# Kernel tuning notes

Measured on AMD Instinct MI355X. Metric: run time of the kernel, lower is better.

Reference implementation:

```python
import jax, jax.numpy as jnp
import numpy as np

B, T, N_EMBD = 1, 512, 768
N_HEAD, N_KV_HEAD = 12, 6
HEAD_DIM = N_EMBD // N_HEAD  # 64


def rms_norm(x, eps=1e-6):
    return x * jax.lax.rsqrt(jnp.mean(x * x, axis=-1, keepdims=True) + eps)


def apply_rotary_emb(x, cos, sin):
    # x: [B, T, H, D]; cos/sin: [T, D//2]
    d2 = x.shape[-1] // 2
    x1, x2 = x[..., :d2], x[..., d2:]
    c = cos[None, :, None, :]
    s = sin[None, :, None, :]
    return jnp.concatenate([x1 * c - x2 * s, x2 * c + x1 * s], axis=-1)


def tropical_dot_product(q, k):
    # q: [B,H,T,D], k: [B,H,S,D] -> max-plus score [B,H,T,S]
    return jnp.max(q[..., :, None, :] + k[..., None, :, :], axis=-1)


def setup_inputs() -> dict:
    key = jax.random.key(0)
    ks = jax.random.split(key, 5)
    x = jax.random.normal(ks[0], (B, T, N_EMBD), dtype=jnp.float32)
    # Real RoPE tables
    half = HEAD_DIM // 2
    inv_freq = 1.0 / (10000.0 ** (np.arange(0, half, dtype=np.float32) / half))
    t = np.arange(T, dtype=np.float32)
    freqs = np.outer(t, inv_freq)  # [T, D//2]
    cos = jnp.asarray(np.cos(freqs), dtype=jnp.float32)
    sin = jnp.asarray(np.sin(freqs), dtype=jnp.float32)
    std = 0.02
    Wq = std * jax.random.normal(ks[1], (N_EMBD, N_HEAD * HEAD_DIM), dtype=jnp.float32)
    Wk = std * jax.random.normal(ks[2], (N_EMBD, N_KV_HEAD * HEAD_DIM), dtype=jnp.float32)
    Wv = std * jax.random.normal(ks[3], (N_EMBD, N_KV_HEAD * HEAD_DIM), dtype=jnp.float32)
    Wproj = std * jax.random.normal(ks[4], (N_EMBD, N_EMBD), dtype=jnp.float32)
    return {"x": x, "cos": cos, "sin": sin, "Wq": Wq, "Wk": Wk, "Wv": Wv, "Wproj": Wproj}


def reference(x, cos, sin, Wq, Wk, Wv, Wproj):
    b, t, c = x.shape
    q = (x @ Wq).reshape(b, t, N_HEAD, HEAD_DIM)
    k = (x @ Wk).reshape(b, t, N_KV_HEAD, HEAD_DIM)
    v = (x @ Wv).reshape(b, t, N_KV_HEAD, HEAD_DIM)
    q = rms_norm(apply_rotary_emb(q, cos, sin))
    k = rms_norm(apply_rotary_emb(k, cos, sin))
    q = jnp.transpose(q, (0, 2, 1, 3))  # [B,H,T,D]
    k = jnp.transpose(k, (0, 2, 1, 3))  # [B,Hkv,T,D]
    v = jnp.transpose(v, (0, 2, 1, 3))
    n_rep = N_HEAD // N_KV_HEAD
    if n_rep > 1:
        k = jnp.repeat(k, n_rep, axis=1)
        v = jnp.repeat(v, n_rep, axis=1)
    scores = tropical_dot_product(q, k)  # [B,H,T,T]
    causal = jnp.tril(jnp.ones((t, t), dtype=jnp.bool_))
    scores = scores + jnp.where(causal, 0.0, -jnp.inf)
    attn = jax.nn.softmax(scores, axis=-1)
    y = jnp.einsum('bhqk,bhkd->bhqd', attn, v)
    y = jnp.transpose(y, (0, 2, 1, 3)).reshape(b, t, c)
    return y @ Wproj
```

## Files before the change

kernel.cpp:

```cpp
#include <hip/hip_runtime.h>
#include <hip/hip_bf16.h>
#include <math.h>

#define TT   512
#define CEMB 768
#define NH   12
#define NKV  6
#define HD   64
#define KVC  (NKV*HD)

typedef short short8 __attribute__((ext_vector_type(8)));
typedef float floatx4 __attribute__((ext_vector_type(4)));
typedef float floatx2 __attribute__((ext_vector_type(2)));

__device__ __forceinline__ unsigned pack_bf16(float lo, float hi){
  __hip_bfloat162 h = __float22bfloat162_rn(make_float2(lo, hi));
  return *reinterpret_cast<unsigned*>(&h);
}
__device__ __forceinline__ unsigned short bf16_rn(float f){
  unsigned u = __float_as_uint(f);
  u += 0x7FFFu + ((u>>16)&1u);
  return (unsigned short)(u>>16);
}
__device__ __forceinline__ float bf16_to_f32(unsigned short u){
  return __uint_as_float(((unsigned)u) << 16);
}

__global__ void __launch_bounds__(256) gemm_qkv_mfma(
    const float* __restrict__ X,
    const float* __restrict__ Wq, const float* __restrict__ Wk, const float* __restrict__ Wv,
    const float* __restrict__ Wp,
    const float* __restrict__ cosb, const float* __restrict__ sinb,
    float* __restrict__ q, float* __restrict__ k, float* __restrict__ v,
    unsigned short* __restrict__ WpF){
  int bx = blockIdx.x;
  if (bx >= 192){
    int t0 = (bx-192)*256 + threadIdx.x;
    for(int g=0; g<8; ++g){
      int u  = g*9216 + t0;
      int kp = u / 192;
      int n4 = (u - kp*192)*4;
      int kk = kp*2;
      float4 w0 = *(const float4*)&Wp[(size_t)kk*CEMB + n4];
      float4 w1 = *(const float4*)&Wp[(size_t)(kk+1)*CEMB + n4];
      int ks = kk>>5, qq = (kk>>3)&3, j = kk&7;
      #pragma unroll
      for(int i=0;i<4;i++){
        int n = n4+i, ct = n>>4, r = n&15;
        *(unsigned*)&WpF[ (((size_t)(ct*24 + ks)*64 + qq*16 + r)<<3) + j ] =
          pack_bf16((&w0.x)[i], (&w1.x)[i]);
      }
    }
    return;
  }
  int mt = bx / 24, nt = bx % 24;
  const float* W; int ldb, bcol;
  if (nt < 12)      { W = Wq; ldb = CEMB; bcol = nt*64; }
  else if (nt < 18) { W = Wk; ldb = KVC;  bcol = (nt-12)*64; }
  else              { W = Wv; ldb = KVC;  bcol = (nt-18)*64; }

  __shared__ __align__(16) unsigned short Al[2][64][40];
  __shared__ __align__(16) unsigned short Bl[2][64][40];

  int tid = threadIdx.x;
  int am  = tid>>2,  akg = (tid&3)*8;
  int bkp = tid>>4,  bn4 = (tid&15)*4;
  int w = tid>>6, lane = tid&63, qq = lane>>4, r = lane&15;

  floatx4 acc[4];
  #pragma unroll
  for(int c=0;c<4;c++) acc[c] = (floatx4){0.f,0.f,0.f,0.f};

  const float* Ap = X + (size_t)(mt*64 + am)*CEMB + akg;
  const float* Bp = W + (size_t)(2*bkp)*ldb + bcol + bn4;

  float4 a00 = *(const float4*)(Ap);
  float4 a01 = *(const float4*)(Ap + 4);
  float4 b00 = *(const float4*)(Bp);
  float4 b01 = *(const float4*)(Bp + ldb);
  float4 a10 = *(const float4*)(Ap + 32);
  float4 a11 = *(const float4*)(Ap + 36);
  float4 b10 = *(const float4*)(Bp + (size_t)32*ldb);
  float4 b11 = *(const float4*)(Bp + (size_t)33*ldb);

  auto step = [&](int k0, float4& A0, float4& A1, float4& B0, float4& B1,
                  int bufc) {
    unsigned p0 = pack_bf16(A0.x,A0.y), p1 = pack_bf16(A0.z,A0.w);
    unsigned p2 = pack_bf16(A1.x,A1.y), p3 = pack_bf16(A1.z,A1.w);
    *(uint4*)&Al[bufc][am][akg] = make_uint4(p0,p1,p2,p3);
    #pragma unroll
    for(int i=0;i<4;i++)
      *(unsigned*)&Bl[bufc][bn4+i][2*bkp] = pack_bf16((&B0.x)[i], (&B1.x)[i]);
    if (k0 + 64 < CEMB){
      A0 = *(const float4*)(Ap + k0+64);
      A1 = *(const float4*)(Ap + k0+68);
      B0 = *(const float4*)(Bp + (size_t)(k0+64)*ldb);
      B1 = *(const float4*)(Bp + (size_t)(k0+65)*ldb);
    }
    __syncthreads();
    short8 af = *(short8*)&Al[bufc][w*16 + r][qq*8];
    #pragma unroll
    for(int c=0;c<4;c++){
      short8 bfr = *(short8*)&Bl[bufc][c*16 + r][qq*8];
      acc[c] = __builtin_amdgcn_mfma_f32_16x16x32_bf16(af, bfr, acc[c], 0,0,0);
    }
  };

  for(int k0=0; k0<CEMB; k0+=64){
    step(k0,    a00,a01,b00,b01, 0);
    step(k0+32, a10,a11,b10,b11, 1);
  }

  #pragma unroll
  for(int reg=0; reg<4; ++reg){
    int t = mt*64 + w*16 + qq*4 + reg;
    if (nt < 18){
      float cs0 = cosb[t*32 + r],      sn0 = sinb[t*32 + r];
      float cs1 = cosb[t*32 + 16 + r], sn1 = sinb[t*32 + 16 + r];
      float x0 = acc[0][reg], x1 = acc[1][reg], x2 = acc[2][reg], x3 = acc[3][reg];
      float n0 = x0*cs0 - x2*sn0;
      float n1 = x1*cs1 - x3*sn1;
      float n2 = x2*cs0 + x0*sn0;
      float n3 = x3*cs1 + x1*sn1;
      float ss = n0*n0 + n1*n1 + n2*n2 + n3*n3;
      ss += __shfl_xor(ss,1); ss += __shfl_xor(ss,2);
      ss += __shfl_xor(ss,4); ss += __shfl_xor(ss,8);
      float sc = rsqrtf(ss*(1.0f/64.0f) + 1e-6f);
      float* dst = (nt < 12) ? (q + (size_t)t*CEMB + nt*64)
                             : (k + (size_t)t*KVC + (nt-12)*64);
      dst[r]    = n0*sc; dst[16+r] = n1*sc;
      dst[32+r] = n2*sc; dst[48+r] = n3*sc;
    } else {
      float* dst = v + (size_t)t*KVC + (nt-18)*64;
      dst[r]    = acc[0][reg]; dst[16+r] = acc[1][reg];
      dst[32+r] = acc[2][reg]; dst[48+r] = acc[3][reg];
    }
  }
}

__global__ void __launch_bounds__(256) attn_tile(const float* __restrict__ qn,
    const float* __restrict__ kn, const float* __restrict__ vr,
    unsigned short* __restrict__ part_acc, float2* __restrict__ part_ml){
  __shared__ float QPsh[32*68];
  __shared__ float Ksh[64*64];
  __shared__ float Vsh[64*64];

  int h   = blockIdx.y;
  int idx = blockIdx.x;
  int qs = 0, rem = idx;
  while (rem > (qs>>1)){ rem -= (qs>>1)+1; ++qs; }
  int ct = rem;
  int t0 = ct*64;

  int kvh  = h >> 1;
  int tid  = threadIdx.x;
  int w    = tid >> 6;
  int lane = tid & 63;
  int lg   = lane >> 4;
  int lc   = lane & 15;

  {
    int rr = tid >> 4;
    int c4 = (tid & 15) * 4;
    *(float4*)&QPsh[rr*68 + c4] =
      *(const float4*)&qn[(size_t)(qs*32+rr)*CEMB + h*HD + c4];
    *(float4*)&QPsh[(rr+16)*68 + c4] =
      *(const float4*)&qn[(size_t)(qs*32+rr+16)*CEMB + h*HD + c4];
  }
  #pragma unroll
  for(int sub=0; sub<4; ++sub){
    int rr = w*16 + sub*4 + lg;
    int sw = ((lc ^ (rr>>2)) & 15)*4;
    *(float4*)&Ksh[rr*64 + sw] =
      *(const float4*)&kn[(size_t)(t0+rr)*KVC + kvh*HD + lc*4];
    *(float4*)&Vsh[rr*64 + sw] =
      *(const float4*)&vr[(size_t)(t0+rr)*KVC + kvh*HD + lc*4];
  }
  __syncthreads();

  float s[2][4];
  #pragma unroll
  for(int r=0;r<2;r++)
    #pragma unroll
    for(int c=0;c<4;c++) s[r][c] = -INFINITY;

  #pragma unroll
  for(int dg=0; dg<16; ++dg){
    floatx2 ka[4], kb[4];
    int ksw = ((dg ^ lc)&15)*4;
    #pragma unroll
    for(int c=0;c<4;c++){
      float4 kv = *(const float4*)&Ksh[(lc*4+c)*64 + ksw];
      ka[c] = (floatx2){kv.x, kv.y};
      kb[c] = (floatx2){kv.z, kv.w};
    }
    #pragma unroll
    for(int r=0;r<2;r++){
      float4 qv = *(const float4*)&QPsh[(w*8+lg*2+r)*68 + dg*4];
      floatx2 qa = (floatx2){qv.x, qv.y};
      floatx2 qb = (floatx2){qv.z, qv.w};
      #pragma unroll
      for(int c=0;c<4;c++){
        floatx2 sa = qa + ka[c];
        floatx2 sb = qb + kb[c];
        s[r][c] = fmaxf(s[r][c],
                  fmaxf(fmaxf(sa.x, sa.y), fmaxf(sb.x, sb.y)));
      }
    }
  }

  float mrow[2], lrow[2];
  #pragma unroll
  for(int r=0;r<2;r++){
    int i = qs*32 + w*8 + lg*2 + r;
    #pragma unroll
    for(int c=0;c<4;c++)
      if (t0 + lc*4 + c > i) s[r][c] = -INFINITY;
    float mt = fmaxf(fmaxf(s[r][0],s[r][1]), fmaxf(s[r][2],s[r][3]));
    mt = fmaxf(mt, __shfl_xor(mt,1));
    mt = fmaxf(mt, __shfl_xor(mt,2));
    mt = fmaxf(mt, __shfl_xor(mt,4));
    mt = fmaxf(mt, __shfl_xor(mt,8));
    float p0 = __expf(s[r][0]-mt), p1 = __expf(s[r][1]-mt);
    float p2 = __expf(s[r][2]-mt), p3 = __expf(s[r][3]-mt);
    float ps = p0+p1+p2+p3;
    ps += __shfl_xor(ps,1); ps += __shfl_xor(ps,2);
    ps += __shfl_xor(ps,4); ps += __shfl_xor(ps,8);
    mrow[r] = mt; lrow[r] = ps;
    *(float4*)&QPsh[(w*8+lg*2+r)*68 + lc*4] = make_float4(p0,p1,p2,p3);
  }
  __builtin_amdgcn_wave_barrier();

  floatx2 acc2[2][2];
  #pragma unroll
  for(int r=0;r<2;r++){
    acc2[r][0] = (floatx2){0.f,0.f};
    acc2[r][1] = (floatx2){0.f,0.f};
  }

  #pragma unroll
  for(int jg=0; jg<16; ++jg){
    floatx2 va[4], vb[4];
    int vsw = ((lc ^ jg)&15)*4;
    #pragma unroll
    for(int jj=0;jj<4;jj++){
      float4 vv = *(const float4*)&Vsh[(jg*4+jj)*64 + vsw];
      va[jj] = (floatx2){vv.x, vv.y};
      vb[jj] = (floatx2){vv.z, vv.w};
    }
    #pragma unroll
    for(int r=0;r<2;r++){
      float4 pv = *(const float4*)&QPsh[(w*8+lg*2+r)*68 + jg*4];
      #pragma unroll
      for(int jj=0;jj<4;jj++){
        float pj = (&pv.x)[jj];
        floatx2 pp = (floatx2){pj, pj};
        acc2[r][0] = __builtin_elementwise_fma(pp, va[jj], acc2[r][0]);
        acc2[r][1] = __builtin_elementwise_fma(pp, vb[jj], acc2[r][1]);
      }
    }
  }

  #pragma unroll
  for(int r=0;r<2;r++){
    int i = qs*32 + w*8 + lg*2 + r;
    int pidx = (h*TT + i)*8 + ct;
    *(uint2*)&part_acc[(size_t)pidx*64 + lc*4] =
      make_uint2(pack_bf16(acc2[r][0].x, acc2[r][0].y),
                 pack_bf16(acc2[r][1].x, acc2[r][1].y));
    if (lc == 0) part_ml[pidx] = make_float2(mrow[r], lrow[r]);
  }
}

__global__ void __launch_bounds__(256) attn_reduce(const unsigned short* __restrict__ part_acc,
    const float2* __restrict__ part_ml, unsigned short* __restrict__ yF){
  int wid  = (blockIdx.x * blockDim.x + threadIdx.x) >> 6;
  int lane = threadIdx.x & 63;
  int h = wid >> 9;
  int i = wid & 511;
  int nch = (i >> 6) + 1;
  int base = (h*TT + i)*8;

  float2 mls[8]; float acs[8];
  #pragma unroll
  for(int c=0;c<8;c++){
    mls[c] = part_ml[base + c];
    acs[c] = bf16_to_f32(part_acc[(size_t)(base + c)*64 + lane]);
  }

  float m = -INFINITY, l = 0.f, a = 0.f;
  #pragma unroll
  for(int c=0;c<8;c++){
    if (c < nch){
      float m_new = fmaxf(m, mls[c].x);
      float sa  = __expf(m - m_new);
      float sc_ = __expf(mls[c].x - m_new);
      l = l*sa + mls[c].y*sc_;
      a = a*sa + acs[c]*sc_;
      m = m_new;
    }
  }
  float val = a / l;
  int s = i>>4, rr = i&15;
  int ks = h*2 + (lane>>5), q2 = (lane>>3)&3, j = lane&7;
  yF[ (((size_t)(s*24 + ks)*64 + q2*16 + rr)<<3) + j ] = bf16_rn(val);
}

__global__ void __launch_bounds__(256) gemm_proj_mfma(
    const unsigned short* __restrict__ yF, const unsigned short* __restrict__ WpF,
    float* __restrict__ out){
  int bx = blockIdx.x;
  int mt = bx / 24, ntH = bx % 24;
  int tid = threadIdx.x, w = tid>>6, lane = tid&63, qq = lane>>4, r = lane&15;
  int s = mt*4 + w;

  const short8* Af = (const short8*)yF  + (size_t)s*24*64 + lane;
  const short8* Bf = (const short8*)WpF + lane;

  floatx4 acc[2];
  acc[0] = (floatx4){0.f,0.f,0.f,0.f};
  acc[1] = (floatx4){0.f,0.f,0.f,0.f};

  short8 ar[4]; short8 br[4][2];
  #pragma unroll
  for(int j=0;j<3;++j){
    ar[j] = Af[(size_t)j*64];
    #pragma unroll
    for(int c=0;c<2;c++) br[j][c] = Bf[(size_t)((ntH*2+c)*24 + j)*64];
  }

  #pragma unroll
  for(int ks=0; ks<24; ++ks){
    int cur = ks & 3;
    if (ks + 3 < 24){
      int nx = (ks+3) & 3;
      ar[nx] = Af[(size_t)(ks+3)*64];
      #pragma unroll
      for(int c=0;c<2;c++) br[nx][c] = Bf[(size_t)((ntH*2+c)*24 + ks+3)*64];
    }
    #pragma unroll
    for(int c=0;c<2;c++)
      acc[c] = __builtin_amdgcn_mfma_f32_16x16x32_bf16(ar[cur], br[cur][c], acc[c], 0,0,0);
  }

  #pragma unroll
  for(int reg=0; reg<4; ++reg){
    int t = mt*64 + w*16 + qq*4 + reg;
    float* dst = out + (size_t)t*CEMB + ntH*32;
    #pragma unroll
    for(int c=0;c<2;c++)
      dst[c*16 + r] = acc[c][reg];
  }
}

extern "C" void kernel_launch(void* const* d_in, const int* in_sizes, int n_in,
                              void* d_out, int out_size, void* d_ws, size_t ws_size,
                              hipStream_t stream){
  const float* x    = (const float*)d_in[0];
  const float* cosb = (const float*)d_in[1];
  const float* sinb = (const float*)d_in[2];
  const float* Wq   = (const float*)d_in[3];
  const float* Wk   = (const float*)d_in[4];
  const float* Wv   = (const float*)d_in[5];
  const float* Wp   = (const float*)d_in[6];
  float* out = (float*)d_out;

  float* ws        = (float*)d_ws;
  float* q_raw     = ws;
  float* k_raw     = q_raw + (size_t)TT*CEMB;
  float* v_raw     = k_raw + (size_t)TT*KVC;
  unsigned short* part_acc = (unsigned short*)(v_raw + (size_t)TT*KVC);
  float2* part_ml  = (float2*)(part_acc + (size_t)NH*TT*8*64);
  unsigned short* WpF = (unsigned short*)(part_ml + (size_t)NH*TT*8);
  unsigned short* yF  = WpF + (size_t)48*24*64*8;

  gemm_qkv_mfma <<<dim3(228),   256, 0, stream>>>(x, Wq, Wk, Wv, Wp, cosb, sinb,
                                                  q_raw, k_raw, v_raw, WpF);
  attn_tile     <<<dim3(72,NH), 256, 0, stream>>>(q_raw, k_raw, v_raw, part_acc, part_ml);
  attn_reduce   <<<dim3(NH*TT/4), 256, 0, stream>>>(part_acc, part_ml, yF);
  gemm_proj_mfma<<<dim3(192),   256, 0, stream>>>(yF, WpF, out);
}
```

Before: 116.1 us.

## Enlarge attention tile to 64 query rows with 2 waves and 8 rows per thread

The attention tile kernel now processes 64 query rows per block instead of 32, using 128 threads where each thread computes 8 rows instead of 2. Every K/V element loaded from LDS is therefore reused across more query rows, and the launch shrinks from 72 to 36 blocks per head. The aim is to cut LDS traffic and redundant K/V loads per unit of work. The cost is higher register pressure, fewer blocks in flight (432 total on a chip with many CUs), and some wasted causal work on diagonal tiles.

```diff
diff --git a/kernel.cpp b/kernel.cpp
--- a/kernel.cpp
+++ b/kernel.cpp
@@ -138,39 +138,33 @@
   }
 }
 
-__global__ void __launch_bounds__(256) attn_tile(const float* __restrict__ qn,
+__global__ void __launch_bounds__(128) attn_tile(const float* __restrict__ qn,
     const float* __restrict__ kn, const float* __restrict__ vr,
     unsigned short* __restrict__ part_acc, float2* __restrict__ part_ml){
-  __shared__ float QPsh[32*68];
+  __shared__ float QPsh[64*68];
   __shared__ float Ksh[64*64];
   __shared__ float Vsh[64*64];
 
   int h   = blockIdx.y;
   int idx = blockIdx.x;
-  int qs = 0, rem = idx;
-  while (rem > (qs>>1)){ rem -= (qs>>1)+1; ++qs; }
+  int qt = 0, rem = idx;
+  while (rem > qt){ rem -= (qt+1); ++qt; }
   int ct = rem;
   int t0 = ct*64;
 
   int kvh  = h >> 1;
   int tid  = threadIdx.x;
-  int w    = tid >> 6;
+  int wv   = tid >> 6;
   int lane = tid & 63;
   int lg   = lane >> 4;
   int lc   = lane & 15;
 
-  {
-    int rr = tid >> 4;
-    int c4 = (tid & 15) * 4;
-    *(float4*)&QPsh[rr*68 + c4] =
-      *(const float4*)&qn[(size_t)(qs*32+rr)*CEMB + h*HD + c4];
-    *(float4*)&QPsh[(rr+16)*68 + c4] =
-      *(const float4*)&qn[(size_t)(qs*32+rr+16)*CEMB + h*HD + c4];
-  }
-  #pragma unroll
-  for(int sub=0; sub<4; ++sub){
-    int rr = w*16 + sub*4 + lg;
+  #pragma unroll
+  for(int sub=0; sub<8; ++sub){
+    int rr = wv*32 + sub*4 + lg;
     int sw = ((lc ^ (rr>>2)) & 15)*4;
+    *(float4*)&QPsh[rr*68 + lc*4] =
+      *(const float4*)&qn[(size_t)(qt*64+rr)*CEMB + h*HD + lc*4];
     *(float4*)&Ksh[rr*64 + sw] =
       *(const float4*)&kn[(size_t)(t0+rr)*KVC + kvh*HD + lc*4];
     *(float4*)&Vsh[rr*64 + sw] =
@@ -178,9 +172,12 @@
   }
   __syncthreads();
 
-  float s[2][4];
-  #pragma unroll
-  for(int r=0;r<2;r++)
+  int rbase = wv*32 + lg*2;
+  #define RLOC(r) (rbase + ((r)>>1)*8 + ((r)&1))
+
+  float s[8][4];
+  #pragma unroll
+  for(int r=0;r<8;r++)
     #pragma unroll
     for(int c=0;c<4;c++) s[r][c] = -INFINITY;
 
@@ -195,8 +192,8 @@
       kb[c] = (floatx2){kv.z, kv.w};
     }
     #pragma unroll
-    for(int r=0;r<2;r++){
-      float4 qv = *(const float4*)&QPsh[(w*8+lg*2+r)*68 + dg*4];
+    for(int r=0;r<8;r++){
+      float4 qv = *(const float4*)&QPsh[RLOC(r)*68 + dg*4];
       floatx2 qa = (floatx2){qv.x, qv.y};
       floatx2 qb = (floatx2){qv.z, qv.w};
       #pragma unroll
@@ -209,10 +206,10 @@
     }
   }
 
-  float mrow[2], lrow[2];
-  #pragma unroll
-  for(int r=0;r<2;r++){
-    int i = qs*32 + w*8 + lg*2 + r;
+  float mrow[8], lrow[8];
+  #pragma unroll
+  for(int r=0;r<8;r++){
+    int i = qt*64 + RLOC(r);
     #pragma unroll
     for(int c=0;c<4;c++)
       if (t0 + lc*4 + c > i) s[r][c] = -INFINITY;
@@ -227,15 +224,15 @@
     ps += __shfl_xor(ps,1); ps += __shfl_xor(ps,2);
     ps += __shfl_xor(ps,4); ps += __shfl_xor(ps,8);
     mrow[r] = mt; lrow[r] = ps;
-    *(float4*)&QPsh[(w*8+lg*2+r)*68 + lc*4] = make_float4(p0,p1,p2,p3);
+    *(float4*)&QPsh[RLOC(r)*68 + lc*4] = make_float4(p0,p1,p2,p3);
   }
   __builtin_amdgcn_wave_barrier();
 
-  floatx2 acc2[2][2];
-  #pragma unroll
-  for(int r=0;r<2;r++){
-    acc2[r][0] = (floatx2){0.f,0.f};
-    acc2[r][1] = (floatx2){0.f,0.f};
+  floatx2 a0[8], a1[8];
+  #pragma unroll
+  for(int r=0;r<8;r++){
+    a0[r] = (floatx2){0.f,0.f};
+    a1[r] = (floatx2){0.f,0.f};
   }
 
   #pragma unroll
@@ -249,27 +246,28 @@
       vb[jj] = (floatx2){vv.z, vv.w};
     }
     #pragma unroll
-    for(int r=0;r<2;r++){
-      float4 pv = *(const float4*)&QPsh[(w*8+lg*2+r)*68 + jg*4];
+    for(int r=0;r<8;r++){
+      float4 pv = *(const float4*)&QPsh[RLOC(r)*68 + jg*4];
       #pragma unroll
       for(int jj=0;jj<4;jj++){
         float pj = (&pv.x)[jj];
         floatx2 pp = (floatx2){pj, pj};
-        acc2[r][0] = __builtin_elementwise_fma(pp, va[jj], acc2[r][0]);
-        acc2[r][1] = __builtin_elementwise_fma(pp, vb[jj], acc2[r][1]);
+        a0[r] = __builtin_elementwise_fma(pp, va[jj], a0[r]);
+        a1[r] = __builtin_elementwise_fma(pp, vb[jj], a1[r]);
       }
     }
   }
 
   #pragma unroll
-  for(int r=0;r<2;r++){
-    int i = qs*32 + w*8 + lg*2 + r;
+  for(int r=0;r<8;r++){
+    int i = qt*64 + RLOC(r);
     int pidx = (h*TT + i)*8 + ct;
     *(uint2*)&part_acc[(size_t)pidx*64 + lc*4] =
-      make_uint2(pack_bf16(acc2[r][0].x, acc2[r][0].y),
-                 pack_bf16(acc2[r][1].x, acc2[r][1].y));
+      make_uint2(pack_bf16(a0[r].x, a0[r].y),
+                 pack_bf16(a1[r].x, a1[r].y));
     if (lc == 0) part_ml[pidx] = make_float2(mrow[r], lrow[r]);
   }
+  #undef RLOC
 }
 
 __global__ void __launch_bounds__(256) attn_reduce(const unsigned short* __restrict__ part_acc,
@@ -376,7 +374,7 @@
 
   gemm_qkv_mfma <<<dim3(228),   256, 0, stream>>>(x, Wq, Wk, Wv, Wp, cosb, sinb,
                                                   q_raw, k_raw, v_raw, WpF);
-  attn_tile     <<<dim3(72,NH), 256, 0, stream>>>(q_raw, k_raw, v_raw, part_acc, part_ml);
+  attn_tile     <<<dim3(36,NH), 128, 0, stream>>>(q_raw, k_raw, v_raw, part_acc, part_ml);
   attn_reduce   <<<dim3(NH*TT/4), 256, 0, stream>>>(part_acc, part_ml, yF);
   gemm_proj_mfma<<<dim3(192),   256, 0, stream>>>(yF, WpF, out);
 }
```

Result: slower. 140.3 us (+20.9%).
